# Kernel optimization log

Hardware: AMD Instinct MI355X
Metric: run time of the kernel (lower is better)

Reference implementation:

```python
import jax, jax.numpy as jnp
import numpy as np

C = 128   # in_channels
K = 7     # local attention kernel_size
B, H, W = 1, 128, 128
PAD = K // 2


def conv_bn(x, w, s, b, relu=True):
    # 1x1 conv (no bias) + folded eval-mode BatchNorm (per-channel scale/bias)
    y = jnp.einsum('bchw,oc->bohw', x, w)
    y = y * s[None, :, None, None] + b[None, :, None, None]
    return jax.nn.relu(y) if relu else y


def local_attention(q, k, v, ksize):
    # q,k,v: (B,C,H,W). Windowed self-attention over ksize x ksize neighborhood
    # (equivalent to F.unfold(key/value, ksize, padding=ksize//2) + dot + softmax + weighted sum)
    pad = ksize // 2
    kp = jnp.pad(k, ((0, 0), (0, 0), (pad, pad), (pad, pad)))
    vp = jnp.pad(v, ((0, 0), (0, 0), (pad, pad), (pad, pad)))
    Hh, Ww = q.shape[2], q.shape[3]
    offsets = [(i, j) for i in range(ksize) for j in range(ksize)]
    # sim: (B, k*k, H, W) -- dot over channels per window offset
    sim = jnp.stack([jnp.einsum('bchw,bchw->bhw', q, kp[:, :, i:i + Hh, j:j + Ww])
                     for (i, j) in offsets], axis=1)
    attn = jax.nn.softmax(sim, axis=1)
    out = jnp.zeros_like(q)
    for idx, (i, j) in enumerate(offsets):
        out = out + attn[:, idx][:, None] * vp[:, :, i:i + Hh, j:j + Ww]
    return out


def setup_inputs() -> dict:
    key = jax.random.key(0)
    ks = jax.random.split(key, 19)
    d = {'x': jax.random.normal(ks[0], (B, C, H, W), jnp.float32)}
    names = ['q1', 'q2', 'k1', 'k2', 'v', 'o']
    for idx, n in enumerate(names):
        cin = 2 * C if n == 'o' else C
        kw, ksc, kb = ks[1 + 3 * idx], ks[2 + 3 * idx], ks[3 + 3 * idx]
        d['w_' + n] = jax.random.normal(kw, (C, cin), jnp.float32) / np.sqrt(cin).astype(np.float32)
        d['s_' + n] = jax.random.uniform(ksc, (C,), jnp.float32, 0.5, 1.5)
        d['b_' + n] = jax.random.normal(kb, (C,), jnp.float32) * 0.1
    return d


def reference(x, w_q1, s_q1, b_q1, w_q2, s_q2, b_q2,
              w_k1, s_k1, b_k1, w_k2, s_k2, b_k2,
              w_v, s_v, b_v, w_o, s_o, b_o):
    # query/key projections: two ConvBNReLU 1x1; value: one ConvBNReLU 1x1
    q = conv_bn(conv_bn(x, w_q1, s_q1, b_q1), w_q2, s_q2, b_q2)
    k = conv_bn(conv_bn(x, w_k1, s_k1, b_k1), w_k2, s_k2, b_k2)
    v = conv_bn(x, w_v, s_v, b_v)
    new_feat = local_attention(q, k, v, K)
    # integration: cat([attn_out, x], dim=1) -> 1x1 conv + BN (no activation)
    cat = jnp.concatenate([new_feat, x], axis=1)  # (B, 2C, H, W)
    return conv_bn(cat, w_o, s_o, b_o, relu=False)
```

## Files before the change

### kernel.cpp

```cpp
#include <hip/hip_runtime.h>


typedef short short8 __attribute__((ext_vector_type(8)));
typedef short short4v __attribute__((ext_vector_type(4)));
typedef float f32x4 __attribute__((ext_vector_type(4)));

#define HW_PIX 16384
#define CH 128
#define PADW 134
#define PSLOT (134 * 134 * 128)

#define WQ1_OFF 0
#define WQ2_OFF 16384
#define WK1_OFF 32768
#define WK2_OFF 49152
#define WV_OFF  65536
#define WO_OFF  81920
#define SB_OFF  114688
#define TQ_OFF  117760
#define XT_OFF  (TQ_OFF + 2097152)
#define KP_OFF  (XT_OFF + 2097152)
#define VP_OFF  (KP_OFF + PSLOT)

static __device__ __forceinline__ float bf2f(unsigned short u) {
    union { unsigned int i; float f; } c; c.i = ((unsigned int)u) << 16; return c.f;
}
static __device__ __forceinline__ unsigned short f2bf(float f) {
    union { unsigned int i; float f; } c; c.f = f;
    unsigned int x = c.i;
    return (unsigned short)((x + 0x7fffu + ((x >> 16) & 1u)) >> 16);
}

struct CvtArgs { const float* w[6]; const float* sb[12]; };

__global__ __launch_bounds__(256)
void cvt_k(CvtArgs a, short* __restrict__ ws)
{
    const int u = blockIdx.x * 256 + threadIdx.x;
    if (u < 14336) {
        const int s0 = u * 8;
        const int seg = (s0 < 81920) ? (s0 >> 14) : 5;
        const int base = (seg < 5) ? (seg << 14) : 81920;
        const float* fp = a.w[seg] + (s0 - base);
        short8 o;
        #pragma unroll
        for (int j = 0; j < 8; ++j) o[j] = (short)f2bf(fp[j]);
        *(short8*)(ws + s0) = o;
    } else if (u < 15872) {
        const int idx = u - 14336;
        ((float*)(ws + SB_OFF))[idx] = a.sb[idx >> 7][idx & 127];
    } else if (u < 15872 + 3144) {
        const int idx = u - 15872;
        const int buf = idx / 1572;
        const int e   = idx % 1572;
        int row, col;
        if (e < 402)      { row = e / PADW;          col = e % PADW; }
        else if (e < 804) { row = 131 + (e - 402) / PADW; col = (e - 402) % PADW; }
        else { const int r = e - 804; row = 3 + r / 6; const int c = r % 6;
               col = (c < 3) ? c : (128 + c); }
        short* p = ws + (buf ? VP_OFF : KP_OFF) + (row * PADW + col) * CH;
        const short8 z = {0, 0, 0, 0, 0, 0, 0, 0};
        #pragma unroll
        for (int j = 0; j < 16; ++j) *(short8*)(p + j * 8) = z;
    }
}

__global__ __launch_bounds__(256)
void qkv_k(const float* __restrict__ x, short* __restrict__ ws)
{
    const float* sb = (const float*)(ws + SB_OFF);
    const int tid = threadIdx.x;
    const int bid = blockIdx.x;
    const int t   = (bid & 7) * 128 + (bid >> 3);
    const int tr = t >> 5, tc = t & 31;
    const int h0 = tr * 4, w0 = tc * 4;

    const int l16 = tid & 15;
    const int g   = (tid & 63) >> 4;
    const int wv  = tid >> 6;
    const int o0  = wv * 32;

    __shared__ short xb[16 * 136];
    __shared__ short tileQ[16 * 136];
    __shared__ short tileK[16 * 136];
    __shared__ short tileV[16 * 136];

    #pragma unroll
    for (int pass = 0; pass < 2; ++pass) {
        const int u = tid + pass * 256;
        const int c = u >> 2, r = u & 3;
        f32x4 v = *(const f32x4*)(x + c * HW_PIX + (h0 + r) * 128 + w0);
        #pragma unroll
        for (int j = 0; j < 4; ++j) xb[(r * 4 + j) * 136 + c] = (short)f2bf(v[j]);
    }
    __syncthreads();

    {
        const int px = tid >> 4, c8 = tid & 15;
        const int p_img = (h0 + (px >> 2)) * 128 + w0 + (px & 3);
        *(short8*)(ws + XT_OFF + p_img * CH + c8 * 8) =
            *(const short8*)(xb + px * 136 + c8 * 8);
    }

    short8 xa[4];
    #pragma unroll
    for (int kk = 0; kk < 4; ++kk)
        xa[kk] = *(const short8*)(xb + l16 * 136 + kk * 32 + g * 8);

    const f32x4 z = {0.f, 0.f, 0.f, 0.f};
    f32x4 acc[2];

    #define GEMM1(WOFF, SIDX, TILE)                                              \
    {                                                                            \
        acc[0] = z; acc[1] = z;                                                  \
        _Pragma("unroll")                                                        \
        for (int kk = 0; kk < 4; ++kk) {                                         \
            _Pragma("unroll")                                                    \
            for (int nt = 0; nt < 2; ++nt) {                                     \
                short8 bv = *(const short8*)(ws + WOFF +                         \
                    (o0 + nt * 16 + l16) * 128 + kk * 32 + g * 8);               \
                acc[nt] = __builtin_amdgcn_mfma_f32_16x16x32_bf16(xa[kk], bv, acc[nt], 0, 0, 0); \
            }                                                                    \
        }                                                                        \
        _Pragma("unroll")                                                        \
        for (int nt = 0; nt < 2; ++nt) {                                         \
            const int o = o0 + nt * 16 + l16;                                    \
            const float sf = sb[(SIDX) * 128 + o], bf = sb[(SIDX + 1) * 128 + o];\
            _Pragma("unroll")                                                    \
            for (int i = 0; i < 4; ++i) {                                        \
                const float vl = fmaxf(acc[nt][i] * sf + bf, 0.f);               \
                TILE[(g * 4 + i) * 136 + o] = (short)f2bf(vl);                   \
            }                                                                    \
        }                                                                        \
    }
    GEMM1(WQ1_OFF, 0, tileQ)
    GEMM1(WK1_OFF, 4, tileK)
    GEMM1(WV_OFF,  8, tileV)
    #undef GEMM1

    __syncthreads();

    short8 lf[4];
    f32x4 accQ[2], accK[2];
    accQ[0] = z; accQ[1] = z; accK[0] = z; accK[1] = z;
    #pragma unroll
    for (int kk = 0; kk < 4; ++kk) lf[kk] = *(const short8*)(tileQ + l16 * 136 + kk * 32 + g * 8);
    #pragma unroll
    for (int kk = 0; kk < 4; ++kk) {
        #pragma unroll
        for (int nt = 0; nt < 2; ++nt) {
            short8 bv = *(const short8*)(ws + WQ2_OFF + (o0 + nt * 16 + l16) * 128 + kk * 32 + g * 8);
            accQ[nt] = __builtin_amdgcn_mfma_f32_16x16x32_bf16(lf[kk], bv, accQ[nt], 0, 0, 0);
        }
    }
    #pragma unroll
    for (int kk = 0; kk < 4; ++kk) lf[kk] = *(const short8*)(tileK + l16 * 136 + kk * 32 + g * 8);
    #pragma unroll
    for (int kk = 0; kk < 4; ++kk) {
        #pragma unroll
        for (int nt = 0; nt < 2; ++nt) {
            short8 bv = *(const short8*)(ws + WK2_OFF + (o0 + nt * 16 + l16) * 128 + kk * 32 + g * 8);
            accK[nt] = __builtin_amdgcn_mfma_f32_16x16x32_bf16(lf[kk], bv, accK[nt], 0, 0, 0);
        }
    }
    __syncthreads();

    #pragma unroll
    for (int nt = 0; nt < 2; ++nt) {
        const int o = o0 + nt * 16 + l16;
        const float sfq = sb[2 * 128 + o], bfq = sb[3 * 128 + o];
        const float sfk = sb[6 * 128 + o], bfk = sb[7 * 128 + o];
        #pragma unroll
        for (int i = 0; i < 4; ++i) {
            tileQ[(g * 4 + i) * 136 + o] = (short)f2bf(fmaxf(accQ[nt][i] * sfq + bfq, 0.f));
            tileK[(g * 4 + i) * 136 + o] = (short)f2bf(fmaxf(accK[nt][i] * sfk + bfk, 0.f));
        }
    }
    __syncthreads();

    {
        const int px = tid >> 4, c8 = tid & 15;
        const int soff = px * 136 + c8 * 8;
        const int p_img = (h0 + (px >> 2)) * 128 + w0 + (px & 3);
        const int pr = h0 + (px >> 2) + 3, pc = w0 + (px & 3) + 3;
        const int doff = (pr * PADW + pc) * CH + c8 * 8;
        *(short8*)(ws + TQ_OFF + p_img * CH + c8 * 8) = *(const short8*)(tileQ + soff);
        *(short8*)(ws + KP_OFF + doff) = *(const short8*)(tileK + soff);
        *(short8*)(ws + VP_OFF + doff) = *(const short8*)(tileV + soff);
    }
}

__global__ __launch_bounds__(256)
void att_k(const short* __restrict__ ws, float* __restrict__ out)
{
    const float* sb = (const float*)(ws + SB_OFF);

    __shared__ __align__(16) short hal[112 * 128];
    __shared__ __align__(16) short qTl[16 * 136];
    __shared__ __align__(16) short xbl[16 * 136];
    __shared__ __align__(16) short attT[16 * 136];
    __shared__ float Pf[16 * 116];
    __shared__ float rzL[16];

    const int tid = threadIdx.x;
    const int bid = blockIdx.x;
    const int t   = (bid & 7) * 128 + (bid >> 3);
    const int tr = t >> 5, tc = t & 31;
    const int h0 = tr * 4, w0 = tc * 4;

    const int l16 = tid & 15;
    const int g   = (tid & 63) >> 4;
    const int wv  = tid >> 6;

    for (int u = tid; u < 1600 + 256; u += 256) {
        if (u < 1600) {
            const int di = u / 160, rem = u - di * 160;
            const int j = rem >> 4, c8 = rem & 15;
            *(short8*)(hal + (di * 10 + j) * 128 + c8 * 8) =
                *(const short8*)(ws + KP_OFF + ((h0 + di) * PADW + (w0 + j)) * CH + c8 * 8);
        } else {
            const int v = u - 1600;
            const int px = v >> 4, c8 = v & 15;
            const int p_img = (h0 + (px >> 2)) * 128 + w0 + (px & 3);
            *(short8*)(qTl + px * 136 + c8 * 8) =
                *(const short8*)(ws + TQ_OFF + p_img * CH + c8 * 8);
        }
    }
    __syncthreads();

    if (wv == 0) {
        short8 af[4];
        #pragma unroll
        for (int kk = 0; kk < 4; ++kk)
            af[kk] = *(const short8*)(qTl + l16 * 136 + kk * 32 + g * 8);

        f32x4 S[7];
        const f32x4 z = {0.f, 0.f, 0.f, 0.f};
        #pragma unroll
        for (int nt = 0; nt < 7; ++nt) S[nt] = z;
        #pragma unroll
        for (int kk = 0; kk < 4; ++kk) {
            #pragma unroll
            for (int nt = 0; nt < 7; ++nt) {
                short8 bv = *(const short8*)(hal + (nt * 16 + l16) * 128 + kk * 32 + g * 8);
                S[nt] = __builtin_amdgcn_mfma_f32_16x16x32_bf16(af[kk], bv, S[nt], 0, 0, 0);
            }
        }
        #pragma unroll
        for (int i = 0; i < 4; ++i) {
            const int px = g * 4 + i;
            const int r = px >> 2, cl = px & 3;
            float vals[7];
            float mx = -3.0e38f;
            #pragma unroll
            for (int nt = 0; nt < 7; ++nt) {
                const int col = nt * 16 + l16;
                const int hr = col / 10, hc = col - hr * 10;
                const bool ok = (col < 100) &&
                                ((unsigned)(hr - r) < 7u) && ((unsigned)(hc - cl) < 7u);
                vals[nt] = ok ? S[nt][i] : -3.0e38f;
                mx = fmaxf(mx, vals[nt]);
            }
            mx = fmaxf(mx, __shfl_xor(mx, 1, 16));
            mx = fmaxf(mx, __shfl_xor(mx, 2, 16));
            mx = fmaxf(mx, __shfl_xor(mx, 4, 16));
            mx = fmaxf(mx, __shfl_xor(mx, 8, 16));
            float zs = 0.f;
            #pragma unroll
            for (int nt = 0; nt < 7; ++nt) {
                const float ev = (vals[nt] > -1.0e37f) ? __expf(vals[nt] - mx) : 0.f;
                zs += ev;
                Pf[px * 116 + nt * 16 + l16] = ev;
            }
            zs += __shfl_xor(zs, 1, 16);
            zs += __shfl_xor(zs, 2, 16);
            zs += __shfl_xor(zs, 4, 16);
            zs += __shfl_xor(zs, 8, 16);
            if (l16 == 0) rzL[px] = 1.0f / zs;
        }
    }
    __syncthreads();

    for (int u = tid; u < 1600 + 256; u += 256) {
        if (u < 1600) {
            const int di = u / 160, rem = u - di * 160;
            const int j = rem >> 4, c8 = rem & 15;
            *(short8*)(hal + (di * 10 + j) * 128 + c8 * 8) =
                *(const short8*)(ws + VP_OFF + ((h0 + di) * PADW + (w0 + j)) * CH + c8 * 8);
        } else {
            const int v = u - 1600;
            const int px = v >> 4, c8 = v & 15;
            const int p_img = (h0 + (px >> 2)) * 128 + w0 + (px & 3);
            *(short8*)(xbl + px * 136 + c8 * 8) =
                *(const short8*)(ws + XT_OFF + p_img * CH + c8 * 8);
        }
    }
    __syncthreads();

    {
        const int px = tid >> 4;
        const int r = px >> 2, cl = px & 3;
        const int cb = l16 * 8;
        float of[8];
        #pragma unroll
        for (int j = 0; j < 8; ++j) of[j] = 0.f;
        #pragma unroll
        for (int off = 0; off < 49; ++off) {
            const int di = off / 7, dj = off % 7;
            const int hp = (r + di) * 10 + cl + dj;
            const float ev = Pf[px * 116 + hp];
            short8 vv = *(const short8*)(hal + hp * 128 + cb);
            #pragma unroll
            for (int j = 0; j < 8; ++j) of[j] += ev * bf2f((unsigned short)vv[j]);
        }
        const float rz = rzL[px];
        short8 ov;
        #pragma unroll
        for (int j = 0; j < 8; ++j) ov[j] = (short)f2bf(of[j] * rz);
        *(short8*)(attT + px * 136 + cb) = ov;
    }
    __syncthreads();

    const int o0 = wv * 32;
    f32x4 fac[2];
    const f32x4 zz = {0.f, 0.f, 0.f, 0.f};
    fac[0] = zz; fac[1] = zz;
    #pragma unroll
    for (int kk = 0; kk < 8; ++kk) {
        const int kbase = kk * 32 + g * 8;
        short8 av;
        if (kk < 4) av = *(const short8*)(attT + l16 * 136 + kbase);
        else        av = *(const short8*)(xbl + l16 * 136 + (kbase - 128));
        #pragma unroll
        for (int nt = 0; nt < 2; ++nt) {
            short8 bv = *(const short8*)(ws + WO_OFF + (o0 + nt * 16 + l16) * 256 + kbase);
            fac[nt] = __builtin_amdgcn_mfma_f32_16x16x32_bf16(av, bv, fac[nt], 0, 0, 0);
        }
    }

    short* outT = hal;
    {
        const float* s  = sb + 10 * 128;
        const float* bb = sb + 11 * 128;
        #pragma unroll
        for (int nt = 0; nt < 2; ++nt) {
            const int o = o0 + nt * 16 + l16;
            const float sf = s[o], bf = bb[o];
            #pragma unroll
            for (int i = 0; i < 4; ++i) {
                const float vl = fac[nt][i] * sf + bf;
                outT[o * 24 + g * 4 + i] = (short)f2bf(vl);
            }
        }
    }
    __syncthreads();
    #pragma unroll
    for (int pass = 0; pass < 2; ++pass) {
        const int u = tid + pass * 256;
        const int c = u >> 2, rr = u & 3;
        short4v sv = *(const short4v*)(outT + c * 24 + rr * 4);
        f32x4 fv;
        #pragma unroll
        for (int j = 0; j < 4; ++j) fv[j] = bf2f((unsigned short)sv[j]);
        *(f32x4*)(out + c * HW_PIX + (h0 + rr) * 128 + w0) = fv;
    }
}

extern "C" void kernel_launch(void* const* d_in, const int* in_sizes, int n_in,
                              void* d_out, int out_size, void* d_ws, size_t ws_size,
                              hipStream_t stream)
{
    const float* x = (const float*)d_in[0];
    short* ws = (short*)d_ws;

    CvtArgs ca;
    ca.w[0] = (const float*)d_in[1];
    ca.w[1] = (const float*)d_in[4];
    ca.w[2] = (const float*)d_in[7];
    ca.w[3] = (const float*)d_in[10];
    ca.w[4] = (const float*)d_in[13];
    ca.w[5] = (const float*)d_in[16];
    ca.sb[0]  = (const float*)d_in[2];  ca.sb[1]  = (const float*)d_in[3];
    ca.sb[2]  = (const float*)d_in[5];  ca.sb[3]  = (const float*)d_in[6];
    ca.sb[4]  = (const float*)d_in[8];  ca.sb[5]  = (const float*)d_in[9];
    ca.sb[6]  = (const float*)d_in[11]; ca.sb[7]  = (const float*)d_in[12];
    ca.sb[8]  = (const float*)d_in[14]; ca.sb[9]  = (const float*)d_in[15];
    ca.sb[10] = (const float*)d_in[17]; ca.sb[11] = (const float*)d_in[18];

    cvt_k<<<dim3(75), dim3(256), 0, stream>>>(ca, ws);
    qkv_k<<<dim3(1024), dim3(256), 0, stream>>>(x, ws);
    att_k<<<dim3(1024), dim3(256), 0, stream>>>(ws, (float*)d_out);
}
```

Before: 62.88 us.

## Fuse projection and attention into one kernel with halo recompute of K/V

Merges the QKV projection and local-attention kernels into a single kernel that loads a padded 10x10 halo of x per 4x4 tile and recomputes the K and V projections for all halo pixels in shared memory. This removes the global workspace round-trip for q, padded k/v and transposed x, along with the zero-padding initialisation and one launch. In exchange, each tile performs several times more K/V projection MFMA work and more barriers, and the x halo gather uses scalar strided loads.

```diff
diff --git a/kernel.cpp b/kernel.cpp
--- a/kernel.cpp
+++ b/kernel.cpp
@@ -7,8 +7,6 @@
 
 #define HW_PIX 16384
 #define CH 128
-#define PADW 134
-#define PSLOT (134 * 134 * 128)
 
 #define WQ1_OFF 0
 #define WQ2_OFF 16384
@@ -17,10 +15,6 @@
 #define WV_OFF  65536
 #define WO_OFF  81920
 #define SB_OFF  114688
-#define TQ_OFF  117760
-#define XT_OFF  (TQ_OFF + 2097152)
-#define KP_OFF  (XT_OFF + 2097152)
-#define VP_OFF  (KP_OFF + PSLOT)
 
 static __device__ __forceinline__ float bf2f(unsigned short u) {
     union { unsigned int i; float f; } c; c.i = ((unsigned int)u) << 16; return c.f;
@@ -49,25 +43,23 @@
     } else if (u < 15872) {
         const int idx = u - 14336;
         ((float*)(ws + SB_OFF))[idx] = a.sb[idx >> 7][idx & 127];
-    } else if (u < 15872 + 3144) {
-        const int idx = u - 15872;
-        const int buf = idx / 1572;
-        const int e   = idx % 1572;
-        int row, col;
-        if (e < 402)      { row = e / PADW;          col = e % PADW; }
-        else if (e < 804) { row = 131 + (e - 402) / PADW; col = (e - 402) % PADW; }
-        else { const int r = e - 804; row = 3 + r / 6; const int c = r % 6;
-               col = (c < 3) ? c : (128 + c); }
-        short* p = ws + (buf ? VP_OFF : KP_OFF) + (row * PADW + col) * CH;
-        const short8 z = {0, 0, 0, 0, 0, 0, 0, 0};
-        #pragma unroll
-        for (int j = 0; j < 16; ++j) *(short8*)(p + j * 8) = z;
     }
 }
 
 __global__ __launch_bounds__(256)
-void qkv_k(const float* __restrict__ x, short* __restrict__ ws)
+void mega_k(const float* __restrict__ x, const short* __restrict__ ws,
+            float* __restrict__ out)
 {
+    __shared__ __align__(16) short xh[100 * 136];
+    __shared__ __align__(16) short kvh[100 * 136];
+    __shared__ __align__(16) short qTa[16 * 136];
+    __shared__ __align__(16) float PT[16 * 100];
+    __shared__ float rzL[16];
+
+    short* tmp  = (short*)PT;
+    short* attT = qTa;
+    short* outT = kvh;
+
     const float* sb = (const float*)(ws + SB_OFF);
     const int tid = threadIdx.x;
     const int bid = blockIdx.x;
@@ -79,220 +71,184 @@
     const int g   = (tid & 63) >> 4;
     const int wv  = tid >> 6;
     const int o0  = wv * 32;
-
-    __shared__ short xb[16 * 136];
-    __shared__ short tileQ[16 * 136];
-    __shared__ short tileK[16 * 136];
-    __shared__ short tileV[16 * 136];
-
-    #pragma unroll
-    for (int pass = 0; pass < 2; ++pass) {
-        const int u = tid + pass * 256;
-        const int c = u >> 2, r = u & 3;
-        f32x4 v = *(const f32x4*)(x + c * HW_PIX + (h0 + r) * 128 + w0);
-        #pragma unroll
-        for (int j = 0; j < 4; ++j) xb[(r * 4 + j) * 136 + c] = (short)f2bf(v[j]);
-    }
-    __syncthreads();
-
-    {
-        const int px = tid >> 4, c8 = tid & 15;
-        const int p_img = (h0 + (px >> 2)) * 128 + w0 + (px & 3);
-        *(short8*)(ws + XT_OFF + p_img * CH + c8 * 8) =
-            *(const short8*)(xb + px * 136 + c8 * 8);
-    }
-
-    short8 xa[4];
-    #pragma unroll
-    for (int kk = 0; kk < 4; ++kk)
-        xa[kk] = *(const short8*)(xb + l16 * 136 + kk * 32 + g * 8);
-
-    const f32x4 z = {0.f, 0.f, 0.f, 0.f};
-    f32x4 acc[2];
-
-    #define GEMM1(WOFF, SIDX, TILE)                                              \
-    {                                                                            \
-        acc[0] = z; acc[1] = z;                                                  \
+    const f32x4 z4 = {0.f, 0.f, 0.f, 0.f};
+
+    #pragma unroll 5
+    for (int it = 0; it < 50; ++it) {
+        const int i = tid + it * 256;
+        const int hr = i / 1280;
+        const int rem = i - hr * 1280;
+        const int c = rem / 10, wc = rem - (rem / 10) * 10;
+        const int hh = h0 - 3 + hr, ww = w0 - 3 + wc;
+        float v = 0.f;
+        if ((unsigned)hh < 128u && (unsigned)ww < 128u)
+            v = x[c * HW_PIX + hh * 128 + ww];
+        xh[(hr * 10 + wc) * 136 + c] = (short)f2bf(v);
+    }
+    __syncthreads();
+
+    #define GEMM32(WOFF)                                                         \
+        acc[0] = z4; acc[1] = z4;                                                \
         _Pragma("unroll")                                                        \
         for (int kk = 0; kk < 4; ++kk) {                                         \
             _Pragma("unroll")                                                    \
             for (int nt = 0; nt < 2; ++nt) {                                     \
                 short8 bv = *(const short8*)(ws + WOFF +                         \
                     (o0 + nt * 16 + l16) * 128 + kk * 32 + g * 8);               \
-                acc[nt] = __builtin_amdgcn_mfma_f32_16x16x32_bf16(xa[kk], bv, acc[nt], 0, 0, 0); \
+                acc[nt] = __builtin_amdgcn_mfma_f32_16x16x32_bf16(af[kk], bv, acc[nt], 0, 0, 0); \
             }                                                                    \
-        }                                                                        \
-        _Pragma("unroll")                                                        \
-        for (int nt = 0; nt < 2; ++nt) {                                         \
-            const int o = o0 + nt * 16 + l16;                                    \
-            const float sf = sb[(SIDX) * 128 + o], bf = sb[(SIDX + 1) * 128 + o];\
-            _Pragma("unroll")                                                    \
-            for (int i = 0; i < 4; ++i) {                                        \
-                const float vl = fmaxf(acc[nt][i] * sf + bf, 0.f);               \
-                TILE[(g * 4 + i) * 136 + o] = (short)f2bf(vl);                   \
-            }                                                                    \
-        }                                                                        \
-    }
-    GEMM1(WQ1_OFF, 0, tileQ)
-    GEMM1(WK1_OFF, 4, tileK)
-    GEMM1(WV_OFF,  8, tileV)
-    #undef GEMM1
-
-    __syncthreads();
-
-    short8 lf[4];
-    f32x4 accQ[2], accK[2];
-    accQ[0] = z; accQ[1] = z; accK[0] = z; accK[1] = z;
-    #pragma unroll
-    for (int kk = 0; kk < 4; ++kk) lf[kk] = *(const short8*)(tileQ + l16 * 136 + kk * 32 + g * 8);
-    #pragma unroll
-    for (int kk = 0; kk < 4; ++kk) {
-        #pragma unroll
-        for (int nt = 0; nt < 2; ++nt) {
-            short8 bv = *(const short8*)(ws + WQ2_OFF + (o0 + nt * 16 + l16) * 128 + kk * 32 + g * 8);
-            accQ[nt] = __builtin_amdgcn_mfma_f32_16x16x32_bf16(lf[kk], bv, accQ[nt], 0, 0, 0);
-        }
-    }
-    #pragma unroll
-    for (int kk = 0; kk < 4; ++kk) lf[kk] = *(const short8*)(tileK + l16 * 136 + kk * 32 + g * 8);
-    #pragma unroll
-    for (int kk = 0; kk < 4; ++kk) {
-        #pragma unroll
-        for (int nt = 0; nt < 2; ++nt) {
-            short8 bv = *(const short8*)(ws + WK2_OFF + (o0 + nt * 16 + l16) * 128 + kk * 32 + g * 8);
-            accK[nt] = __builtin_amdgcn_mfma_f32_16x16x32_bf16(lf[kk], bv, accK[nt], 0, 0, 0);
-        }
-    }
-    __syncthreads();
-
+        }
+
+    const int qrow = 33 + (l16 >> 2) * 10 + (l16 & 3);
+    short8 af[4];
+    f32x4 acc[2];
+
+    #pragma unroll
+    for (int kk = 0; kk < 4; ++kk)
+        af[kk] = *(const short8*)(xh + qrow * 136 + kk * 32 + g * 8);
+    GEMM32(WQ1_OFF)
     #pragma unroll
     for (int nt = 0; nt < 2; ++nt) {
         const int o = o0 + nt * 16 + l16;
-        const float sfq = sb[2 * 128 + o], bfq = sb[3 * 128 + o];
-        const float sfk = sb[6 * 128 + o], bfk = sb[7 * 128 + o];
-        #pragma unroll
-        for (int i = 0; i < 4; ++i) {
-            tileQ[(g * 4 + i) * 136 + o] = (short)f2bf(fmaxf(accQ[nt][i] * sfq + bfq, 0.f));
-            tileK[(g * 4 + i) * 136 + o] = (short)f2bf(fmaxf(accK[nt][i] * sfk + bfk, 0.f));
+        const float sf = sb[0 * 128 + o], bf = sb[1 * 128 + o];
+        #pragma unroll
+        for (int i = 0; i < 4; ++i)
+            tmp[(g * 4 + i) * 136 + o] = (short)f2bf(fmaxf(acc[nt][i] * sf + bf, 0.f));
+    }
+    __syncthreads();
+
+    #pragma unroll
+    for (int kk = 0; kk < 4; ++kk)
+        af[kk] = *(const short8*)(tmp + l16 * 136 + kk * 32 + g * 8);
+    GEMM32(WQ2_OFF)
+    #pragma unroll
+    for (int nt = 0; nt < 2; ++nt) {
+        const int o = o0 + nt * 16 + l16;
+        const float sf = sb[2 * 128 + o], bf = sb[3 * 128 + o];
+        #pragma unroll
+        for (int i = 0; i < 4; ++i)
+            qTa[(g * 4 + i) * 136 + o] = (short)f2bf(fmaxf(acc[nt][i] * sf + bf, 0.f));
+    }
+    __syncthreads();
+
+    for (int m = 0; m < 7; ++m) {
+        int arow = m * 16 + l16; if (arow > 99) arow = 99;
+        #pragma unroll
+        for (int kk = 0; kk < 4; ++kk)
+            af[kk] = *(const short8*)(xh + arow * 136 + kk * 32 + g * 8);
+        GEMM32(WK1_OFF)
+        #pragma unroll
+        for (int nt = 0; nt < 2; ++nt) {
+            const int o = o0 + nt * 16 + l16;
+            const float sf = sb[4 * 128 + o], bf = sb[5 * 128 + o];
+            #pragma unroll
+            for (int i = 0; i < 4; ++i)
+                tmp[(g * 4 + i) * 136 + o] = (short)f2bf(fmaxf(acc[nt][i] * sf + bf, 0.f));
+        }
+        __syncthreads();
+        #pragma unroll
+        for (int kk = 0; kk < 4; ++kk)
+            af[kk] = *(const short8*)(tmp + l16 * 136 + kk * 32 + g * 8);
+        GEMM32(WK2_OFF)
+        #pragma unroll
+        for (int nt = 0; nt < 2; ++nt) {
+            const int o = o0 + nt * 16 + l16;
+            const float sf = sb[6 * 128 + o], bf = sb[7 * 128 + o];
+            #pragma unroll
+            for (int i = 0; i < 4; ++i) {
+                const int px = m * 16 + g * 4 + i;
+                if (px < 100) {
+                    const int hr = px / 10, hc = px - (px / 10) * 10;
+                    const bool okimg = ((unsigned)(h0 - 3 + hr) < 128u) &&
+                                       ((unsigned)(w0 - 3 + hc) < 128u);
+                    const float vl = okimg ? fmaxf(acc[nt][i] * sf + bf, 0.f) : 0.f;
+                    kvh[px * 136 + o] = (short)f2bf(vl);
+                }
+            }
+        }
+        __syncthreads();
+    }
+
+    #pragma unroll
+    for (int kk = 0; kk < 4; ++kk)
+        af[kk] = *(const short8*)(qTa + l16 * 136 + kk * 32 + g * 8);
+    #pragma unroll
+    for (int s = 0; s < 2; ++s) {
+        const int nt = wv + s * 4;
+        if (nt < 7) {
+            f32x4 sa = z4;
+            #pragma unroll
+            for (int kk = 0; kk < 4; ++kk) {
+                short8 bv = *(const short8*)(kvh + (nt * 16 + l16) * 136 + kk * 32 + g * 8);
+                sa = __builtin_amdgcn_mfma_f32_16x16x32_bf16(af[kk], bv, sa, 0, 0, 0);
+            }
+            const int col = nt * 16 + l16;
+            if (col < 100) {
+                #pragma unroll
+                for (int i = 0; i < 4; ++i)
+                    PT[(g * 4 + i) * 100 + col] = sa[i];
+            }
         }
     }
     __syncthreads();
 
     {
-        const int px = tid >> 4, c8 = tid & 15;
-        const int soff = px * 136 + c8 * 8;
-        const int p_img = (h0 + (px >> 2)) * 128 + w0 + (px & 3);
-        const int pr = h0 + (px >> 2) + 3, pc = w0 + (px & 3) + 3;
-        const int doff = (pr * PADW + pc) * CH + c8 * 8;
-        *(short8*)(ws + TQ_OFF + p_img * CH + c8 * 8) = *(const short8*)(tileQ + soff);
-        *(short8*)(ws + KP_OFF + doff) = *(const short8*)(tileK + soff);
-        *(short8*)(ws + VP_OFF + doff) = *(const short8*)(tileV + soff);
-    }
-}
-
-__global__ __launch_bounds__(256)
-void att_k(const short* __restrict__ ws, float* __restrict__ out)
-{
-    const float* sb = (const float*)(ws + SB_OFF);
-
-    __shared__ __align__(16) short hal[112 * 128];
-    __shared__ __align__(16) short qTl[16 * 136];
-    __shared__ __align__(16) short xbl[16 * 136];
-    __shared__ __align__(16) short attT[16 * 136];
-    __shared__ float Pf[16 * 116];
-    __shared__ float rzL[16];
-
-    const int tid = threadIdx.x;
-    const int bid = blockIdx.x;
-    const int t   = (bid & 7) * 128 + (bid >> 3);
-    const int tr = t >> 5, tc = t & 31;
-    const int h0 = tr * 4, w0 = tc * 4;
-
-    const int l16 = tid & 15;
-    const int g   = (tid & 63) >> 4;
-    const int wv  = tid >> 6;
-
-    for (int u = tid; u < 1600 + 256; u += 256) {
-        if (u < 1600) {
-            const int di = u / 160, rem = u - di * 160;
-            const int j = rem >> 4, c8 = rem & 15;
-            *(short8*)(hal + (di * 10 + j) * 128 + c8 * 8) =
-                *(const short8*)(ws + KP_OFF + ((h0 + di) * PADW + (w0 + j)) * CH + c8 * 8);
-        } else {
-            const int v = u - 1600;
-            const int px = v >> 4, c8 = v & 15;
-            const int p_img = (h0 + (px >> 2)) * 128 + w0 + (px & 3);
-            *(short8*)(qTl + px * 136 + c8 * 8) =
-                *(const short8*)(ws + TQ_OFF + p_img * CH + c8 * 8);
-        }
-    }
-    __syncthreads();
-
-    if (wv == 0) {
-        short8 af[4];
+        const int px = tid >> 4;
+        const int r = px >> 2, cl = px & 3;
+        float vals[7];
+        float mx = -3.0e38f;
+        #pragma unroll
+        for (int n = 0; n < 7; ++n) {
+            const int hp = n * 16 + l16;
+            float v = -3.0e38f;
+            if (hp < 100) {
+                const int hr = hp / 10, hc = hp - (hp / 10) * 10;
+                if ((unsigned)(hr - r) < 7u && (unsigned)(hc - cl) < 7u)
+                    v = PT[px * 100 + hp];
+            }
+            vals[n] = v; mx = fmaxf(mx, v);
+        }
+        mx = fmaxf(mx, __shfl_xor(mx, 1, 16));
+        mx = fmaxf(mx, __shfl_xor(mx, 2, 16));
+        mx = fmaxf(mx, __shfl_xor(mx, 4, 16));
+        mx = fmaxf(mx, __shfl_xor(mx, 8, 16));
+        float zs = 0.f;
+        #pragma unroll
+        for (int n = 0; n < 7; ++n) {
+            const int hp = n * 16 + l16;
+            const float ev = (vals[n] > -1.0e37f) ? __expf(vals[n] - mx) : 0.f;
+            zs += ev;
+            if (hp < 100) PT[px * 100 + hp] = ev;
+        }
+        zs += __shfl_xor(zs, 1, 16);
+        zs += __shfl_xor(zs, 2, 16);
+        zs += __shfl_xor(zs, 4, 16);
+        zs += __shfl_xor(zs, 8, 16);
+        if (l16 == 0) rzL[px] = 1.0f / zs;
+    }
+    __syncthreads();
+
+    for (int m = 0; m < 7; ++m) {
+        int arow = m * 16 + l16; if (arow > 99) arow = 99;
         #pragma unroll
         for (int kk = 0; kk < 4; ++kk)
-            af[kk] = *(const short8*)(qTl + l16 * 136 + kk * 32 + g * 8);
-
-        f32x4 S[7];
-        const f32x4 z = {0.f, 0.f, 0.f, 0.f};
-        #pragma unroll
-        for (int nt = 0; nt < 7; ++nt) S[nt] = z;
-        #pragma unroll
-        for (int kk = 0; kk < 4; ++kk) {
-            #pragma unroll
-            for (int nt = 0; nt < 7; ++nt) {
-                short8 bv = *(const short8*)(hal + (nt * 16 + l16) * 128 + kk * 32 + g * 8);
-                S[nt] = __builtin_amdgcn_mfma_f32_16x16x32_bf16(af[kk], bv, S[nt], 0, 0, 0);
-            }
-        }
-        #pragma unroll
-        for (int i = 0; i < 4; ++i) {
-            const int px = g * 4 + i;
-            const int r = px >> 2, cl = px & 3;
-            float vals[7];
-            float mx = -3.0e38f;
-            #pragma unroll
-            for (int nt = 0; nt < 7; ++nt) {
-                const int col = nt * 16 + l16;
-                const int hr = col / 10, hc = col - hr * 10;
-                const bool ok = (col < 100) &&
-                                ((unsigned)(hr - r) < 7u) && ((unsigned)(hc - cl) < 7u);
-                vals[nt] = ok ? S[nt][i] : -3.0e38f;
-                mx = fmaxf(mx, vals[nt]);
-            }
-            mx = fmaxf(mx, __shfl_xor(mx, 1, 16));
-            mx = fmaxf(mx, __shfl_xor(mx, 2, 16));
-            mx = fmaxf(mx, __shfl_xor(mx, 4, 16));
-            mx = fmaxf(mx, __shfl_xor(mx, 8, 16));
-            float zs = 0.f;
-            #pragma unroll
-            for (int nt = 0; nt < 7; ++nt) {
-                const float ev = (vals[nt] > -1.0e37f) ? __expf(vals[nt] - mx) : 0.f;
-                zs += ev;
-                Pf[px * 116 + nt * 16 + l16] = ev;
-            }
-            zs += __shfl_xor(zs, 1, 16);
-            zs += __shfl_xor(zs, 2, 16);
-            zs += __shfl_xor(zs, 4, 16);
-            zs += __shfl_xor(zs, 8, 16);
-            if (l16 == 0) rzL[px] = 1.0f / zs;
-        }
-    }
-    __syncthreads();
-
-    for (int u = tid; u < 1600 + 256; u += 256) {
-        if (u < 1600) {
-            const int di = u / 160, rem = u - di * 160;
-            const int j = rem >> 4, c8 = rem & 15;
-            *(short8*)(hal + (di * 10 + j) * 128 + c8 * 8) =
-                *(const short8*)(ws + VP_OFF + ((h0 + di) * PADW + (w0 + j)) * CH + c8 * 8);
-        } else {
-            const int v = u - 1600;
-            const int px = v >> 4, c8 = v & 15;
-            const int p_img = (h0 + (px >> 2)) * 128 + w0 + (px & 3);
-            *(short8*)(xbl + px * 136 + c8 * 8) =
-                *(const short8*)(ws + XT_OFF + p_img * CH + c8 * 8);
+            af[kk] = *(const short8*)(xh + arow * 136 + kk * 32 + g * 8);
+        GEMM32(WV_OFF)
+        #pragma unroll
+        for (int nt = 0; nt < 2; ++nt) {
+            const int o = o0 + nt * 16 + l16;
+            const float sf = sb[8 * 128 + o], bf = sb[9 * 128 + o];
+            #pragma unroll
+            for (int i = 0; i < 4; ++i) {
+                const int px = m * 16 + g * 4 + i;
+                if (px < 100) {
+                    const int hr = px / 10, hc = px - (px / 10) * 10;
+                    const bool okimg = ((unsigned)(h0 - 3 + hr) < 128u) &&
+                                       ((unsigned)(w0 - 3 + hc) < 128u);
+                    const float vl = okimg ? fmaxf(acc[nt][i] * sf + bf, 0.f) : 0.f;
+                    kvh[px * 136 + o] = (short)f2bf(vl);
+                }
+            }
         }
     }
     __syncthreads();
@@ -308,8 +264,8 @@
         for (int off = 0; off < 49; ++off) {
             const int di = off / 7, dj = off % 7;
             const int hp = (r + di) * 10 + cl + dj;
-            const float ev = Pf[px * 116 + hp];
-            short8 vv = *(const short8*)(hal + hp * 128 + cb);
+            const float ev = PT[px * 100 + hp];
+            short8 vv = *(const short8*)(kvh + hp * 136 + cb);
             #pragma unroll
             for (int j = 0; j < 8; ++j) of[j] += ev * bf2f((unsigned short)vv[j]);
         }
@@ -321,24 +277,20 @@
     }
     __syncthreads();
 
-    const int o0 = wv * 32;
     f32x4 fac[2];
-    const f32x4 zz = {0.f, 0.f, 0.f, 0.f};
-    fac[0] = zz; fac[1] = zz;
+    fac[0] = z4; fac[1] = z4;
     #pragma unroll
     for (int kk = 0; kk < 8; ++kk) {
         const int kbase = kk * 32 + g * 8;
         short8 av;
         if (kk < 4) av = *(const short8*)(attT + l16 * 136 + kbase);
-        else        av = *(const short8*)(xbl + l16 * 136 + (kbase - 128));
+        else        av = *(const short8*)(xh + qrow * 136 + (kbase - 128));
         #pragma unroll
         for (int nt = 0; nt < 2; ++nt) {
             short8 bv = *(const short8*)(ws + WO_OFF + (o0 + nt * 16 + l16) * 256 + kbase);
             fac[nt] = __builtin_amdgcn_mfma_f32_16x16x32_bf16(av, bv, fac[nt], 0, 0, 0);
         }
     }
-
-    short* outT = hal;
     {
         const float* s  = sb + 10 * 128;
         const float* bb = sb + 11 * 128;
@@ -347,10 +299,8 @@
             const int o = o0 + nt * 16 + l16;
             const float sf = s[o], bf = bb[o];
             #pragma unroll
-            for (int i = 0; i < 4; ++i) {
-                const float vl = fac[nt][i] * sf + bf;
-                outT[o * 24 + g * 4 + i] = (short)f2bf(vl);
-            }
+            for (int i = 0; i < 4; ++i)
+                outT[o * 24 + g * 4 + i] = (short)f2bf(fac[nt][i] * sf + bf);
         }
     }
     __syncthreads();
@@ -364,6 +314,7 @@
         for (int j = 0; j < 4; ++j) fv[j] = bf2f((unsigned short)sv[j]);
         *(f32x4*)(out + c * HW_PIX + (h0 + rr) * 128 + w0) = fv;
     }
+    #undef GEMM32
 }
 
 extern "C" void kernel_launch(void* const* d_in, const int* in_sizes, int n_in,
@@ -387,7 +338,6 @@
     ca.sb[8]  = (const float*)d_in[14]; ca.sb[9]  = (const float*)d_in[15];
     ca.sb[10] = (const float*)d_in[17]; ca.sb[11] = (const float*)d_in[18];
 
-    cvt_k<<<dim3(75), dim3(256), 0, stream>>>(ca, ws);
-    qkv_k<<<dim3(1024), dim3(256), 0, stream>>>(x, ws);
-    att_k<<<dim3(1024), dim3(256), 0, stream>>>(ws, (float*)d_out);
-}
+    cvt_k<<<dim3(62), dim3(256), 0, stream>>>(ca, ws);
+    mega_k<<<dim3(1024), dim3(256), 0, stream>>>(x, ws, (float*)d_out);
+}
```

Result: slower. 85.36 us (+35.8%).

## Spread QK MFMA and softmax across all waves, shrink and alias LDS

Applied to the files above, without the earlier changes.

The QK score MFMAs, previously done by wave 0 alone, are now split across all four waves, each writing raw scores to LDS. Softmax is then computed by all 256 threads, one 16-lane group per pixel. Q and x tiles are read straight from global memory into registers instead of being staged in LDS. The halo buffer is padded to a 136 stride to cut bank conflicts, and attT/outT alias existing buffers, lowering the LDS footprint to allow higher occupancy. This adds extra barriers and an extra LDS round trip for the scores.

```diff
diff --git a/kernel.cpp b/kernel.cpp
--- a/kernel.cpp
+++ b/kernel.cpp
@@ -195,12 +195,12 @@
 {
     const float* sb = (const float*)(ws + SB_OFF);
 
-    __shared__ __align__(16) short hal[112 * 128];
-    __shared__ __align__(16) short qTl[16 * 136];
-    __shared__ __align__(16) short xbl[16 * 136];
-    __shared__ __align__(16) short attT[16 * 136];
-    __shared__ float Pf[16 * 116];
+    __shared__ __align__(16) short halKV[100 * 136];
+    __shared__ __align__(16) float Pf[16 * 100];
     __shared__ float rzL[16];
+
+    short* attT = (short*)Pf;
+    short* outT = halKV;
 
     const int tid = threadIdx.x;
     const int bid = blockIdx.x;
@@ -211,134 +211,131 @@
     const int l16 = tid & 15;
     const int g   = (tid & 63) >> 4;
     const int wv  = tid >> 6;
-
-    for (int u = tid; u < 1600 + 256; u += 256) {
-        if (u < 1600) {
-            const int di = u / 160, rem = u - di * 160;
-            const int j = rem >> 4, c8 = rem & 15;
-            *(short8*)(hal + (di * 10 + j) * 128 + c8 * 8) =
-                *(const short8*)(ws + KP_OFF + ((h0 + di) * PADW + (w0 + j)) * CH + c8 * 8);
-        } else {
-            const int v = u - 1600;
-            const int px = v >> 4, c8 = v & 15;
-            const int p_img = (h0 + (px >> 2)) * 128 + w0 + (px & 3);
-            *(short8*)(qTl + px * 136 + c8 * 8) =
-                *(const short8*)(ws + TQ_OFF + p_img * CH + c8 * 8);
-        }
-    }
-    __syncthreads();
-
-    if (wv == 0) {
-        short8 af[4];
-        #pragma unroll
-        for (int kk = 0; kk < 4; ++kk)
-            af[kk] = *(const short8*)(qTl + l16 * 136 + kk * 32 + g * 8);
-
-        f32x4 S[7];
-        const f32x4 z = {0.f, 0.f, 0.f, 0.f};
-        #pragma unroll
-        for (int nt = 0; nt < 7; ++nt) S[nt] = z;
-        #pragma unroll
-        for (int kk = 0; kk < 4; ++kk) {
+    const f32x4 z4 = {0.f, 0.f, 0.f, 0.f};
+
+    const int ap_img = (h0 + (l16 >> 2)) * 128 + w0 + (l16 & 3);
+
+    short8 af[4];
+    #pragma unroll
+    for (int kk = 0; kk < 4; ++kk)
+        af[kk] = *(const short8*)(ws + TQ_OFF + ap_img * CH + kk * 32 + g * 8);
+
+    for (int u = tid; u < 1600; u += 256) {
+        const int di = u / 160, rem = u - di * 160;
+        const int j = rem >> 4, c8 = rem & 15;
+        *(short8*)(halKV + (di * 10 + j) * 136 + c8 * 8) =
+            *(const short8*)(ws + KP_OFF + ((h0 + di) * PADW + (w0 + j)) * CH + c8 * 8);
+    }
+    __syncthreads();
+
+    #pragma unroll
+    for (int s = 0; s < 2; ++s) {
+        const int nt = wv + s * 4;
+        if (nt < 7) {
+            f32x4 sa = z4;
             #pragma unroll
-            for (int nt = 0; nt < 7; ++nt) {
-                short8 bv = *(const short8*)(hal + (nt * 16 + l16) * 128 + kk * 32 + g * 8);
-                S[nt] = __builtin_amdgcn_mfma_f32_16x16x32_bf16(af[kk], bv, S[nt], 0, 0, 0);
+            for (int kk = 0; kk < 4; ++kk) {
+                short8 bv = *(const short8*)(halKV + (nt * 16 + l16) * 136 + kk * 32 + g * 8);
+                sa = __builtin_amdgcn_mfma_f32_16x16x32_bf16(af[kk], bv, sa, 0, 0, 0);
             }
-        }
-        #pragma unroll
-        for (int i = 0; i < 4; ++i) {
-            const int px = g * 4 + i;
-            const int r = px >> 2, cl = px & 3;
-            float vals[7];
-            float mx = -3.0e38f;
-            #pragma unroll
-            for (int nt = 0; nt < 7; ++nt) {
-                const int col = nt * 16 + l16;
-                const int hr = col / 10, hc = col - hr * 10;
-                const bool ok = (col < 100) &&
-                                ((unsigned)(hr - r) < 7u) && ((unsigned)(hc - cl) < 7u);
-                vals[nt] = ok ? S[nt][i] : -3.0e38f;
-                mx = fmaxf(mx, vals[nt]);
+            const int col = nt * 16 + l16;
+            if (col < 100) {
+                #pragma unroll
+                for (int i = 0; i < 4; ++i)
+                    Pf[(g * 4 + i) * 100 + col] = sa[i];
             }
-            mx = fmaxf(mx, __shfl_xor(mx, 1, 16));
-            mx = fmaxf(mx, __shfl_xor(mx, 2, 16));
-            mx = fmaxf(mx, __shfl_xor(mx, 4, 16));
-            mx = fmaxf(mx, __shfl_xor(mx, 8, 16));
-            float zs = 0.f;
-            #pragma unroll
-            for (int nt = 0; nt < 7; ++nt) {
-                const float ev = (vals[nt] > -1.0e37f) ? __expf(vals[nt] - mx) : 0.f;
-                zs += ev;
-                Pf[px * 116 + nt * 16 + l16] = ev;
+        }
+    }
+    __syncthreads();
+
+    const int px = tid >> 4;
+    const int r = px >> 2, cl = px & 3;
+    {
+        float vals[7];
+        float mx = -3.0e38f;
+        #pragma unroll
+        for (int n = 0; n < 7; ++n) {
+            const int hp = n * 16 + l16;
+            float v = -3.0e38f;
+            if (hp < 100) {
+                const int hr = hp / 10, hc = hp - (hp / 10) * 10;
+                if ((unsigned)(hr - r) < 7u && (unsigned)(hc - cl) < 7u)
+                    v = Pf[px * 100 + hp];
             }
-            zs += __shfl_xor(zs, 1, 16);
-            zs += __shfl_xor(zs, 2, 16);
-            zs += __shfl_xor(zs, 4, 16);
-            zs += __shfl_xor(zs, 8, 16);
-            if (l16 == 0) rzL[px] = 1.0f / zs;
-        }
-    }
-    __syncthreads();
-
-    for (int u = tid; u < 1600 + 256; u += 256) {
-        if (u < 1600) {
-            const int di = u / 160, rem = u - di * 160;
-            const int j = rem >> 4, c8 = rem & 15;
-            *(short8*)(hal + (di * 10 + j) * 128 + c8 * 8) =
-                *(const short8*)(ws + VP_OFF + ((h0 + di) * PADW + (w0 + j)) * CH + c8 * 8);
-        } else {
-            const int v = u - 1600;
-            const int px = v >> 4, c8 = v & 15;
-            const int p_img = (h0 + (px >> 2)) * 128 + w0 + (px & 3);
-            *(short8*)(xbl + px * 136 + c8 * 8) =
-                *(const short8*)(ws + XT_OFF + p_img * CH + c8 * 8);
-        }
-    }
-    __syncthreads();
-
-    {
-        const int px = tid >> 4;
-        const int r = px >> 2, cl = px & 3;
+            vals[n] = v; mx = fmaxf(mx, v);
+        }
+        mx = fmaxf(mx, __shfl_xor(mx, 1, 16));
+        mx = fmaxf(mx, __shfl_xor(mx, 2, 16));
+        mx = fmaxf(mx, __shfl_xor(mx, 4, 16));
+        mx = fmaxf(mx, __shfl_xor(mx, 8, 16));
+        float zs = 0.f;
+        #pragma unroll
+        for (int n = 0; n < 7; ++n) {
+            const int hp = n * 16 + l16;
+            const float ev = (vals[n] > -1.0e37f) ? __expf(vals[n] - mx) : 0.f;
+            zs += ev;
+            if (hp < 100) Pf[px * 100 + hp] = ev;
+        }
+        zs += __shfl_xor(zs, 1, 16);
+        zs += __shfl_xor(zs, 2, 16);
+        zs += __shfl_xor(zs, 4, 16);
+        zs += __shfl_xor(zs, 8, 16);
+        if (l16 == 0) rzL[px] = 1.0f / zs;
+    }
+    __syncthreads();
+
+    for (int u = tid; u < 1600; u += 256) {
+        const int di = u / 160, rem = u - di * 160;
+        const int j = rem >> 4, c8 = rem & 15;
+        *(short8*)(halKV + (di * 10 + j) * 136 + c8 * 8) =
+            *(const short8*)(ws + VP_OFF + ((h0 + di) * PADW + (w0 + j)) * CH + c8 * 8);
+    }
+    __syncthreads();
+
+    float of[8];
+    {
         const int cb = l16 * 8;
-        float of[8];
         #pragma unroll
         for (int j = 0; j < 8; ++j) of[j] = 0.f;
         #pragma unroll
         for (int off = 0; off < 49; ++off) {
             const int di = off / 7, dj = off % 7;
             const int hp = (r + di) * 10 + cl + dj;
-            const float ev = Pf[px * 116 + hp];
-            short8 vv = *(const short8*)(hal + hp * 128 + cb);
+            const float ev = Pf[px * 100 + hp];
+            short8 vv = *(const short8*)(halKV + hp * 136 + cb);
             #pragma unroll
             for (int j = 0; j < 8; ++j) of[j] += ev * bf2f((unsigned short)vv[j]);
         }
         const float rz = rzL[px];
+        #pragma unroll
+        for (int j = 0; j < 8; ++j) of[j] *= rz;
+    }
+    __syncthreads();
+
+    {
+        const int cb = l16 * 8;
         short8 ov;
         #pragma unroll
-        for (int j = 0; j < 8; ++j) ov[j] = (short)f2bf(of[j] * rz);
+        for (int j = 0; j < 8; ++j) ov[j] = (short)f2bf(of[j]);
         *(short8*)(attT + px * 136 + cb) = ov;
     }
     __syncthreads();
 
     const int o0 = wv * 32;
     f32x4 fac[2];
-    const f32x4 zz = {0.f, 0.f, 0.f, 0.f};
-    fac[0] = zz; fac[1] = zz;
+    fac[0] = z4; fac[1] = z4;
     #pragma unroll
     for (int kk = 0; kk < 8; ++kk) {
         const int kbase = kk * 32 + g * 8;
         short8 av;
         if (kk < 4) av = *(const short8*)(attT + l16 * 136 + kbase);
-        else        av = *(const short8*)(xbl + l16 * 136 + (kbase - 128));
+        else        av = *(const short8*)(ws + XT_OFF + ap_img * CH + (kbase - 128));
         #pragma unroll
         for (int nt = 0; nt < 2; ++nt) {
             short8 bv = *(const short8*)(ws + WO_OFF + (o0 + nt * 16 + l16) * 256 + kbase);
             fac[nt] = __builtin_amdgcn_mfma_f32_16x16x32_bf16(av, bv, fac[nt], 0, 0, 0);
         }
     }
-
-    short* outT = hal;
     {
         const float* s  = sb + 10 * 128;
         const float* bb = sb + 11 * 128;
@@ -347,10 +344,8 @@
             const int o = o0 + nt * 16 + l16;
             const float sf = s[o], bf = bb[o];
             #pragma unroll
-            for (int i = 0; i < 4; ++i) {
-                const float vl = fac[nt][i] * sf + bf;
-                outT[o * 24 + g * 4 + i] = (short)f2bf(vl);
-            }
+            for (int i = 0; i < 4; ++i)
+                outT[o * 24 + g * 4 + i] = (short)f2bf(fac[nt][i] * sf + bf);
         }
     }
     __syncthreads();
```

After: 55.91 us. 1.12x faster.
